# Performance work log

Measured on AMD Instinct MI355X. Metric: run time of the kernel, lower is better.

The kernel has to match this reference:

```python
import jax, jax.numpy as jnp
import numpy as np

B, T, C, E = 4, 4096, 2048, 64

def setup_inputs() -> dict:
    key = jax.random.key(0)
    k1, k2 = jax.random.split(key)
    hidden_states = jax.random.normal(k1, (B, T, C), dtype=jnp.float32)
    sim_matrix = jax.random.normal(k2, (C, E), dtype=jnp.float32)
    gates = jnp.zeros((E,), dtype=jnp.float32)
    return {"hidden_states": hidden_states, "sim_matrix": sim_matrix, "gates": gates}

def reference(hidden_states, sim_matrix, gates):
    b, t, c = hidden_states.shape
    e = sim_matrix.shape[1]
    x = hidden_states.reshape(-1, c)                     # [N, C], N = B*T
    token_affinity = x @ sim_matrix                      # [N, E]
    logits = token_affinity - jax.nn.sigmoid(gates)      # [N, E]
    gated_logits = jax.nn.relu(logits)                   # [N, E]
    mask = (gated_logits > 0).astype(gated_logits.dtype) # STE forward
    inactive = jnp.sum(mask, axis=-1) == 0               # [N]
    fallback_count = jnp.sum(inactive).astype(jnp.float32)
    k_fallback = e // 2
    _, fb_idx = jax.lax.top_k(logits, k_fallback)        # [N, k]
    rows = jnp.arange(x.shape[0])[:, None]
    fb_mask = jnp.zeros_like(mask).at[rows, fb_idx].set(1.0)
    # inactive tokens have all-zero mask, so fallback simply replaces it
    activation_mask = jnp.where(inactive[:, None], fb_mask, mask)
    neg_max = jnp.finfo(gated_logits.dtype).min          # == -finfo.max
    masked = jnp.where(activation_mask > 0, gated_logits, neg_max)
    active_expert_probs = jax.nn.softmax(masked, axis=-1).reshape(b, t, e)
    return (active_expert_probs, fallback_count,
            logits.reshape(b, t, e), activation_mask.reshape(b, t, e))
```

## Files before the change

kernel.cpp:

```cpp
#include <hip/hip_runtime.h>
#include <hip/hip_bf16.h>

#define N_TOK   16384
#define C_DIM   2048
#define E_DIM   64
#define P_OFF   (N_TOK * E_DIM)
#define FB_OFF  P_OFF
#define LG_OFF  (P_OFF + 1)
#define AM_OFF  (2 * P_OFF + 1)

typedef __attribute__((ext_vector_type(8))) short bf16x8;
typedef __attribute__((ext_vector_type(4))) float f32x4;

static __device__ __forceinline__ unsigned short f2bf_rtn(float f) {
    unsigned u = __float_as_uint(f);
    unsigned r = u + 0x7FFFu + ((u >> 16) & 1u);
    return (unsigned short)(r >> 16);
}

__global__ void gating_prepack(const float* __restrict__ sim,
                               unsigned short* __restrict__ Bpk,
                               float* __restrict__ out) {
    int tid = blockIdx.x * 256 + threadIdx.x;
    if (tid == 0) out[FB_OFF] = 0.0f;
    if (tid >= C_DIM * E_DIM) return;
    int k = tid >> 6;
    int e = tid & 63;
    float v = sim[tid];
    int it = k >> 5;
    int gr = (k >> 3) & 3;
    int i  = k & 7;
    int lane = gr * 16 + (e & 15);
    int nb   = e >> 4;
    Bpk[it * 2048 + nb * 512 + lane * 8 + i] = f2bf_rtn(v);
}

__global__ __launch_bounds__(256, 4)
void gating_main(const float* __restrict__ x,
                 const unsigned short* __restrict__ Bpk,
                 const float* __restrict__ gates,
                 float* __restrict__ out) {
    __shared__ float red[4][16][64];

    const int tid = threadIdx.x;
    const int l   = tid & 63;
    const int w   = tid >> 6;
    const int row0 = blockIdx.x * 16;
    const int g    = l >> 4;
    const int e0   = l & 15;
    const float* xr = x + (size_t)(row0 + e0) * C_DIM + w * 512 + g * 8;
    const unsigned short* bw = Bpk + (size_t)w * 16 * 2048 + l * 8;

    f32x4 acc[4];
#pragma unroll
    for (int nb = 0; nb < 4; ++nb) acc[nb] = (f32x4)0.0f;

    bf16x8 Bf[2][4];
#pragma unroll
    for (int b = 0; b < 2; ++b)
#pragma unroll
        for (int f = 0; f < 4; ++f)
            Bf[b][f] = *(const bf16x8*)(bw + b * 2048 + f * 512);
    float4 Ar[4][2];
#pragma unroll
    for (int it = 0; it < 4; ++it) {
        const float* ap = xr + it * 32;
        Ar[it][0] = *(const float4*)ap;
        Ar[it][1] = *(const float4*)(ap + 4);
    }

#pragma unroll
    for (int it = 0; it < 16; ++it) {
        const int sl = it & 3;
        const int bb = it & 1;

        bf16x8 bnx[4];
        if (it < 14) {
            const unsigned short* bp = bw + (it + 2) * 2048;
#pragma unroll
            for (int f = 0; f < 4; ++f)
                bnx[f] = *(const bf16x8*)(bp + f * 512);
        }

        float av[8] = {Ar[sl][0].x, Ar[sl][0].y, Ar[sl][0].z, Ar[sl][0].w,
                       Ar[sl][1].x, Ar[sl][1].y, Ar[sl][1].z, Ar[sl][1].w};

        if (it < 12) {
            const float* ap = xr + (it + 4) * 32;
            Ar[sl][0] = *(const float4*)ap;
            Ar[sl][1] = *(const float4*)(ap + 4);
        }

        bf16x8 ah;
#pragma unroll
        for (int i = 0; i < 8; ++i) ah[i] = (short)f2bf_rtn(av[i]);

#pragma unroll
        for (int nb = 0; nb < 4; ++nb)
            acc[nb] = __builtin_amdgcn_mfma_f32_16x16x32_bf16(ah, Bf[bb][nb], acc[nb], 0, 0, 0);

        if (it < 14) {
#pragma unroll
            for (int f = 0; f < 4; ++f) Bf[bb][f] = bnx[f];
        }
    }

#pragma unroll
    for (int nb = 0; nb < 4; ++nb)
#pragma unroll
        for (int r = 0; r < 4; ++r)
            red[w][nb * 4 + r][l] = acc[nb][r];
    __syncthreads();

    float tot[4];
#pragma unroll
    for (int nb = 0; nb < 4; ++nb)
        tot[nb] = red[0][nb * 4 + w][l] + red[1][nb * 4 + w][l]
                + red[2][nb * 4 + w][l] + red[3][nb * 4 + w][l];

    float sig[4];
#pragma unroll
    for (int nb = 0; nb < 4; ++nb)
        sig[nb] = 1.0f / (1.0f + expf(-gates[nb * 16 + e0]));

    const int t = row0 + g * 4 + w;
    float lg[4];
    bool  act[4];
    int   lcnt = 0;
    float lmax = -3.4e38f;
#pragma unroll
    for (int nb = 0; nb < 4; ++nb) {
        lg[nb]  = tot[nb] - sig[nb];
        act[nb] = lg[nb] > 0.0f;
        if (act[nb]) { lcnt++; lmax = fmaxf(lmax, lg[nb]); }
    }
    int cnt = lcnt;
    float mx = lmax;
#pragma unroll
    for (int m = 1; m < 16; m <<= 1) {
        cnt += __shfl_xor(cnt, m, 16);
        mx   = fmaxf(mx, __shfl_xor(mx, m, 16));
    }

    float p[4], am[4];
    if (cnt > 0) {
        float ex[4], ls = 0.0f;
#pragma unroll
        for (int nb = 0; nb < 4; ++nb) {
            ex[nb] = act[nb] ? expf(lg[nb] - mx) : 0.0f;
            ls += ex[nb];
        }
        float Z = ls;
#pragma unroll
        for (int m = 1; m < 16; m <<= 1) Z += __shfl_xor(Z, m, 16);
        float rz = 1.0f / Z;
#pragma unroll
        for (int nb = 0; nb < 4; ++nb) {
            p[nb]  = ex[nb] * rz;
            am[nb] = act[nb] ? 1.0f : 0.0f;
        }
    } else {
        unsigned selm = 0;
        for (int it = 0; it < 32; ++it) {
            float bv = -3.4e38f;
            int   bi = 127;
#pragma unroll
            for (int nb = 0; nb < 4; ++nb) {
                if (!((selm >> nb) & 1)) {
                    float v = lg[nb];
                    int   e = nb * 16 + e0;
                    if (v > bv || (v == bv && e < bi)) { bv = v; bi = e; }
                }
            }
#pragma unroll
            for (int m = 1; m < 16; m <<= 1) {
                float ov = __shfl_xor(bv, m, 16);
                int   oi = __shfl_xor(bi, m, 16);
                if (ov > bv || (ov == bv && oi < bi)) { bv = ov; bi = oi; }
            }
            if ((bi & 15) == e0) selm |= 1u << (bi >> 4);
        }
#pragma unroll
        for (int nb = 0; nb < 4; ++nb) {
            bool s_ = (selm >> nb) & 1;
            p[nb]  = s_ ? (1.0f / 32.0f) : 0.0f;
            am[nb] = s_ ? 1.0f : 0.0f;
        }
        if (e0 == 0) atomicAdd(&out[FB_OFF], 1.0f);
    }

#pragma unroll
    for (int nb = 0; nb < 4; ++nb) {
        int idx = t * 64 + nb * 16 + e0;
        out[idx]          = p[nb];
        out[LG_OFF + idx] = lg[nb];
        out[AM_OFF + idx] = am[nb];
    }
}

extern "C" void kernel_launch(void* const* d_in, const int* in_sizes, int n_in,
                              void* d_out, int out_size, void* d_ws, size_t ws_size,
                              hipStream_t stream) {
    const float* x     = (const float*)d_in[0];
    const float* sim   = (const float*)d_in[1];
    const float* gates = (const float*)d_in[2];
    float* out = (float*)d_out;
    unsigned short* Bpk = (unsigned short*)d_ws;

    gating_prepack<<<512, 256, 0, stream>>>(sim, Bpk, out);
    gating_main<<<1024, 256, 0, stream>>>(x, Bpk, gates, out);
}
```

Measured before the change: 37.91 us.

## Split GEMM into split-K LDS-staged kernel plus separate epilogue kernel

Replaces the fused kernel with two kernels when workspace allows. The first is a split-K GEMM in which each 512-thread block stages a quarter of the packed bf16 weights in LDS through global_load_lds and computes 128 tokens, writing fp32 partial sums. The second sums the four partials and runs the sigmoid, softmax and fallback top-k epilogue. This is meant to cut repeated global loads of B and to raise memory parallelism. The cost is an extra kernel launch and a 16 MB round trip of partial sums, with the old fused kernel kept as a fallback.

Result: slower. 41.59 us (+9.7%).

```diff
diff --git a/kernel.cpp b/kernel.cpp
--- a/kernel.cpp
+++ b/kernel.cpp
@@ -8,6 +8,9 @@
 #define FB_OFF  P_OFF
 #define LG_OFF  (P_OFF + 1)
 #define AM_OFF  (2 * P_OFF + 1)
+
+#define BPK_BYTES  262144
+#define PART_BYTES ((size_t)4 * N_TOK * E_DIM * 4)
 
 typedef __attribute__((ext_vector_type(8))) short bf16x8;
 typedef __attribute__((ext_vector_type(4))) float f32x4;
@@ -35,8 +38,184 @@
     Bpk[it * 2048 + nb * 512 + lane * 8 + i] = f2bf_rtn(v);
 }
 
+__global__ __launch_bounds__(512, 4)
+void gating_gemm(const float* __restrict__ x,
+                 const unsigned short* __restrict__ Bpk,
+                 float* __restrict__ part) {
+    __shared__ unsigned short Blds[32768];
+
+    const int tid = threadIdx.x;
+    const int kq  = blockIdx.x & 3;
+    const int tg  = blockIdx.x >> 2;
+
+    const unsigned short* bq = Bpk + kq * 32768;
+#pragma unroll
+    for (int j = 0; j < 8; ++j) {
+        __builtin_amdgcn_global_load_lds(
+            (const __attribute__((address_space(1))) unsigned int*)(bq + j * 4096 + tid * 8),
+            (__attribute__((address_space(3))) unsigned int*)(&Blds[j * 4096 + tid * 8]),
+            16, 0, 0);
+    }
+    __syncthreads();
+
+    const int l   = tid & 63;
+    const int w   = tid >> 6;
+    const int g   = l >> 4;
+    const int e0  = l & 15;
+    const int trow0 = tg * 128 + w * 16;
+    const float* xr = x + (size_t)(trow0 + e0) * C_DIM + kq * 512 + g * 8;
+
+    f32x4 acc[4];
+#pragma unroll
+    for (int nb = 0; nb < 4; ++nb) acc[nb] = (f32x4)0.0f;
+
+    float4 Ac[2][2][2];
+#pragma unroll
+    for (int st = 0; st < 2; ++st) {
+        const float* ap = xr + st * 32;
+        Ac[0][st][0] = *(const float4*)ap;
+        Ac[0][st][1] = *(const float4*)(ap + 4);
+    }
+
+#pragma unroll
+    for (int c = 0; c < 8; ++c) {
+        const int cur = c & 1, nxt = cur ^ 1;
+        if (c < 7) {
+#pragma unroll
+            for (int st = 0; st < 2; ++st) {
+                const float* ap = xr + ((c + 1) * 2 + st) * 32;
+                Ac[nxt][st][0] = *(const float4*)ap;
+                Ac[nxt][st][1] = *(const float4*)(ap + 4);
+            }
+        }
+#pragma unroll
+        for (int st = 0; st < 2; ++st) {
+            const int it = c * 2 + st;
+            float av[8] = {Ac[cur][st][0].x, Ac[cur][st][0].y,
+                           Ac[cur][st][0].z, Ac[cur][st][0].w,
+                           Ac[cur][st][1].x, Ac[cur][st][1].y,
+                           Ac[cur][st][1].z, Ac[cur][st][1].w};
+            bf16x8 ah;
+#pragma unroll
+            for (int i = 0; i < 8; ++i) ah[i] = (short)f2bf_rtn(av[i]);
+#pragma unroll
+            for (int nb = 0; nb < 4; ++nb) {
+                bf16x8 bf = *(const bf16x8*)(&Blds[it * 2048 + nb * 512 + l * 8]);
+                acc[nb] = __builtin_amdgcn_mfma_f32_16x16x32_bf16(ah, bf, acc[nb], 0, 0, 0);
+            }
+        }
+    }
+
+    float4* pp = (float4*)part;
+#pragma unroll
+    for (int r = 0; r < 4; ++r) {
+        int t = trow0 + g * 4 + r;
+        float4 v = {acc[0][r], acc[1][r], acc[2][r], acc[3][r]};
+        pp[(size_t)(kq * N_TOK + t) * 16 + e0] = v;
+    }
+}
+
 __global__ __launch_bounds__(256, 4)
-void gating_main(const float* __restrict__ x,
+void gating_epi(const float* __restrict__ part,
+                const float* __restrict__ gates,
+                float* __restrict__ out) {
+    const int tid = threadIdx.x;
+    const int l   = tid & 63;
+    const int w   = tid >> 6;
+    const int g   = l >> 4;
+    const int e0  = l & 15;
+    const float4* pp = (const float4*)part;
+
+    float sig[4];
+#pragma unroll
+    for (int nb = 0; nb < 4; ++nb)
+        sig[nb] = 1.0f / (1.0f + expf(-gates[nb * 16 + e0]));
+
+#pragma unroll
+    for (int r = 0; r < 4; ++r) {
+        const int t = blockIdx.x * 64 + w * 16 + g * 4 + r;
+        float4 tot = pp[(size_t)(0 * N_TOK + t) * 16 + e0];
+#pragma unroll
+        for (int s = 1; s < 4; ++s) {
+            float4 v = pp[(size_t)(s * N_TOK + t) * 16 + e0];
+            tot.x += v.x; tot.y += v.y; tot.z += v.z; tot.w += v.w;
+        }
+        float lg[4] = {tot.x - sig[0], tot.y - sig[1], tot.z - sig[2], tot.w - sig[3]};
+        bool  act[4];
+        int   lcnt = 0;
+        float lmax = -3.4e38f;
+#pragma unroll
+        for (int nb = 0; nb < 4; ++nb) {
+            act[nb] = lg[nb] > 0.0f;
+            if (act[nb]) { lcnt++; lmax = fmaxf(lmax, lg[nb]); }
+        }
+        int cnt = lcnt;
+        float mx = lmax;
+#pragma unroll
+        for (int m = 1; m < 16; m <<= 1) {
+            cnt += __shfl_xor(cnt, m, 16);
+            mx   = fmaxf(mx, __shfl_xor(mx, m, 16));
+        }
+
+        float p[4], am[4];
+        if (cnt > 0) {
+            float ex[4], ls = 0.0f;
+#pragma unroll
+            for (int nb = 0; nb < 4; ++nb) {
+                ex[nb] = act[nb] ? expf(lg[nb] - mx) : 0.0f;
+                ls += ex[nb];
+            }
+            float Z = ls;
+#pragma unroll
+            for (int m = 1; m < 16; m <<= 1) Z += __shfl_xor(Z, m, 16);
+            float rz = 1.0f / Z;
+#pragma unroll
+            for (int nb = 0; nb < 4; ++nb) {
+                p[nb]  = ex[nb] * rz;
+                am[nb] = act[nb] ? 1.0f : 0.0f;
+            }
+        } else {
+            unsigned selm = 0;
+            for (int it = 0; it < 32; ++it) {
+                float bv = -3.4e38f;
+                int   bi = 127;
+#pragma unroll
+                for (int nb = 0; nb < 4; ++nb) {
+                    if (!((selm >> nb) & 1)) {
+                        float v = lg[nb];
+                        int   e = nb * 16 + e0;
+                        if (v > bv || (v == bv && e < bi)) { bv = v; bi = e; }
+                    }
+                }
+#pragma unroll
+                for (int m = 1; m < 16; m <<= 1) {
+                    float ov = __shfl_xor(bv, m, 16);
+                    int   oi = __shfl_xor(bi, m, 16);
+                    if (ov > bv || (ov == bv && oi < bi)) { bv = ov; bi = oi; }
+                }
+                if ((bi & 15) == e0) selm |= 1u << (bi >> 4);
+            }
+#pragma unroll
+            for (int nb = 0; nb < 4; ++nb) {
+                bool s_ = (selm >> nb) & 1;
+                p[nb]  = s_ ? (1.0f / 32.0f) : 0.0f;
+                am[nb] = s_ ? 1.0f : 0.0f;
+            }
+            if (e0 == 0) atomicAdd(&out[FB_OFF], 1.0f);
+        }
+
+#pragma unroll
+        for (int nb = 0; nb < 4; ++nb) {
+            int idx = t * 64 + nb * 16 + e0;
+            out[idx]          = p[nb];
+            out[LG_OFF + idx] = lg[nb];
+            out[AM_OFF + idx] = am[nb];
+        }
+    }
+}
+
+__global__ __launch_bounds__(256, 4)
+void gating_mono(const float* __restrict__ x,
                  const unsigned short* __restrict__ Bpk,
                  const float* __restrict__ gates,
                  float* __restrict__ out) {
@@ -73,32 +252,25 @@
     for (int it = 0; it < 16; ++it) {
         const int sl = it & 3;
         const int bb = it & 1;
-
         bf16x8 bnx[4];
         if (it < 14) {
             const unsigned short* bp = bw + (it + 2) * 2048;
 #pragma unroll
-            for (int f = 0; f < 4; ++f)
-                bnx[f] = *(const bf16x8*)(bp + f * 512);
-        }
-
+            for (int f = 0; f < 4; ++f) bnx[f] = *(const bf16x8*)(bp + f * 512);
+        }
         float av[8] = {Ar[sl][0].x, Ar[sl][0].y, Ar[sl][0].z, Ar[sl][0].w,
                        Ar[sl][1].x, Ar[sl][1].y, Ar[sl][1].z, Ar[sl][1].w};
-
         if (it < 12) {
             const float* ap = xr + (it + 4) * 32;
             Ar[sl][0] = *(const float4*)ap;
             Ar[sl][1] = *(const float4*)(ap + 4);
         }
-
         bf16x8 ah;
 #pragma unroll
         for (int i = 0; i < 8; ++i) ah[i] = (short)f2bf_rtn(av[i]);
-
 #pragma unroll
         for (int nb = 0; nb < 4; ++nb)
             acc[nb] = __builtin_amdgcn_mfma_f32_16x16x32_bf16(ah, Bf[bb][nb], acc[nb], 0, 0, 0);
-
         if (it < 14) {
 #pragma unroll
             for (int f = 0; f < 4; ++f) Bf[bb][f] = bnx[f];
@@ -208,5 +380,12 @@
     unsigned short* Bpk = (unsigned short*)d_ws;
 
     gating_prepack<<<512, 256, 0, stream>>>(sim, Bpk, out);
-    gating_main<<<1024, 256, 0, stream>>>(x, Bpk, gates, out);
-}
+
+    if (ws_size >= BPK_BYTES + PART_BYTES) {
+        float* part = (float*)((char*)d_ws + BPK_BYTES);
+        gating_gemm<<<512, 512, 0, stream>>>(x, Bpk, part);
+        gating_epi<<<256, 256, 0, stream>>>(part, gates, out);
+    } else {
+        gating_mono<<<1024, 256, 0, stream>>>(x, Bpk, gates, out);
+    }
+}
```

## Stage activation tiles through swizzled LDS with coalesced row loads

Applied to the files above, without the earlier changes.

Activation loads change from per-lane strided fragment reads to row-contiguous float4 loads, where 16 lanes cover 256 contiguous bytes of a row. The values are converted to bf16 with the hardware conversion intrinsic and written into a double-buffered, XOR-swizzled LDS tile per wave, then read back as MFMA fragments. The aim is better DRAM coalescing on this bandwidth-bound GEMV-like pass, at the cost of extra LDS traffic and register pressure from two in-flight prefetch buffers. The reduction scratch reuses the same shared buffer after a barrier.

After: 36.28 us (median of 2 runs). 4.3% less time.

```diff
diff --git a/kernel.cpp b/kernel.cpp
--- a/kernel.cpp
+++ b/kernel.cpp
@@ -16,6 +16,10 @@
     unsigned u = __float_as_uint(f);
     unsigned r = u + 0x7FFFu + ((u >> 16) & 1u);
     return (unsigned short)(r >> 16);
+}
+static __device__ __forceinline__ unsigned short f2bf_hw(float f) {
+    __hip_bfloat16 h = __float2bfloat16(f);
+    return *reinterpret_cast<unsigned short*>(&h);
 }
 
 __global__ void gating_prepack(const float* __restrict__ sim,
@@ -40,7 +44,7 @@
                  const unsigned short* __restrict__ Bpk,
                  const float* __restrict__ gates,
                  float* __restrict__ out) {
-    __shared__ float red[4][16][64];
+    __shared__ __align__(16) char smem[32768];
 
     const int tid = threadIdx.x;
     const int l   = tid & 63;
@@ -48,63 +52,83 @@
     const int row0 = blockIdx.x * 16;
     const int g    = l >> 4;
     const int e0   = l & 15;
-    const float* xr = x + (size_t)(row0 + e0) * C_DIM + w * 512 + g * 8;
+
+    const int srow = l >> 4;
+    const int scol = l & 15;
+
+    const float* xq = x + (size_t)row0 * C_DIM + w * 512;
+    char* Aw = smem + w * 4096;
+
     const unsigned short* bw = Bpk + (size_t)w * 16 * 2048 + l * 8;
 
     f32x4 acc[4];
 #pragma unroll
     for (int nb = 0; nb < 4; ++nb) acc[nb] = (f32x4)0.0f;
 
+    float4 P[2][4];
+    auto loadA = [&](int ch, int p) {
+#pragma unroll
+        for (int j = 0; j < 4; ++j) {
+            const int row = j * 4 + srow;
+            P[p][j] = *(const float4*)(xq + (size_t)row * C_DIM + ch * 64 + scol * 4);
+        }
+    };
+    auto writeA = [&](int p, int b) {
+        char* dst = Aw + b * 2048;
+#pragma unroll
+        for (int j = 0; j < 4; ++j) {
+            const int row = j * 4 + srow;
+            ushort4 hv;
+            hv.x = f2bf_hw(P[p][j].x); hv.y = f2bf_hw(P[p][j].y);
+            hv.z = f2bf_hw(P[p][j].z); hv.w = f2bf_hw(P[p][j].w);
+            const int wb = (row * 128 + scol * 8) ^ ((row & 7) << 4);
+            *(ushort4*)(dst + wb) = hv;
+        }
+    };
+    auto fragA = [&](int it, int b) -> bf16x8 {
+        const int rb = (e0 * 128 + (it * 4 + g) * 16) ^ ((e0 & 7) << 4);
+        return *(const bf16x8*)(Aw + b * 2048 + rb);
+    };
+
+    loadA(0, 0);
+    writeA(0, 0);
+    loadA(1, 1);
     bf16x8 Bf[2][4];
 #pragma unroll
-    for (int b = 0; b < 2; ++b)
+    for (int b2 = 0; b2 < 2; ++b2)
 #pragma unroll
         for (int f = 0; f < 4; ++f)
-            Bf[b][f] = *(const bf16x8*)(bw + b * 2048 + f * 512);
-    float4 Ar[4][2];
-#pragma unroll
-    for (int it = 0; it < 4; ++it) {
-        const float* ap = xr + it * 32;
-        Ar[it][0] = *(const float4*)ap;
-        Ar[it][1] = *(const float4*)(ap + 4);
-    }
-
-#pragma unroll
-    for (int it = 0; it < 16; ++it) {
-        const int sl = it & 3;
-        const int bb = it & 1;
-
-        bf16x8 bnx[4];
-        if (it < 14) {
-            const unsigned short* bp = bw + (it + 2) * 2048;
-#pragma unroll
-            for (int f = 0; f < 4; ++f)
-                bnx[f] = *(const bf16x8*)(bp + f * 512);
-        }
-
-        float av[8] = {Ar[sl][0].x, Ar[sl][0].y, Ar[sl][0].z, Ar[sl][0].w,
-                       Ar[sl][1].x, Ar[sl][1].y, Ar[sl][1].z, Ar[sl][1].w};
-
-        if (it < 12) {
-            const float* ap = xr + (it + 4) * 32;
-            Ar[sl][0] = *(const float4*)ap;
-            Ar[sl][1] = *(const float4*)(ap + 4);
-        }
-
-        bf16x8 ah;
-#pragma unroll
-        for (int i = 0; i < 8; ++i) ah[i] = (short)f2bf_rtn(av[i]);
-
-#pragma unroll
-        for (int nb = 0; nb < 4; ++nb)
-            acc[nb] = __builtin_amdgcn_mfma_f32_16x16x32_bf16(ah, Bf[bb][nb], acc[nb], 0, 0, 0);
-
-        if (it < 14) {
-#pragma unroll
-            for (int f = 0; f < 4; ++f) Bf[bb][f] = bnx[f];
-        }
-    }
-
+            Bf[b2][f] = *(const bf16x8*)(bw + b2 * 2048 + f * 512);
+
+#pragma unroll
+    for (int ch = 0; ch < 8; ++ch) {
+        const int b = ch & 1;
+
+        bf16x8 af0 = fragA(0, b);
+        bf16x8 af1 = fragA(1, b);
+
+        if (ch < 6) loadA(ch + 2, ch & 1);
+
+#pragma unroll
+        for (int it2 = 0; it2 < 2; ++it2) {
+            const int itg = ch * 2 + it2;
+            const bf16x8 af = it2 ? af1 : af0;
+#pragma unroll
+            for (int nb = 0; nb < 4; ++nb)
+                acc[nb] = __builtin_amdgcn_mfma_f32_16x16x32_bf16(af, Bf[itg & 1][nb], acc[nb], 0, 0, 0);
+            if (itg < 14) {
+                const unsigned short* bp = bw + (itg + 2) * 2048;
+#pragma unroll
+                for (int f = 0; f < 4; ++f)
+                    Bf[itg & 1][f] = *(const bf16x8*)(bp + f * 512);
+            }
+        }
+
+        if (ch < 7) writeA((ch + 1) & 1, b ^ 1);
+    }
+
+    __syncthreads();
+    float (*red)[16][64] = (float(*)[16][64])smem;
 #pragma unroll
     for (int nb = 0; nb < 4; ++nb)
 #pragma unroll
```
